# Performance work log

Hardware: AMD Instinct MI355X
Metric: run time of the kernel (lower is better)

The kernel has to match this reference:

```python
import jax, jax.numpy as jnp
import numpy as np

PATCH = 15  # patch_size (odd, per extract_patches arithmetic)


def _extract_patches(vol, centroids, P):
    """vol: (B,C,H,W,D) float; centroids: (B,N,3) int (x->H, y->W, z->D).
    Returns (B,N,C,P,P,P) with the valid region placed at the patch origin and
    zero padding at the high end of each axis (matches F.pad end-padding)."""
    B, C, H, Wd, D = vol.shape
    half = P // 2
    c = centroids.astype(jnp.int32)                      # (B,N,3)
    dims = jnp.array([H, Wd, D], dtype=jnp.int32)
    starts = jnp.maximum(c - half, 0)                    # (B,N,3)
    ends = jnp.minimum(c + half + 1, dims)               # (B,N,3)
    r = jnp.arange(P, dtype=jnp.int32)
    idx = starts[..., None] + r                          # (B,N,3,P)
    mask = idx < ends[..., None]                         # (B,N,3,P)
    idxc = jnp.minimum(idx, (dims - 1)[None, None, :, None])  # clamp for safe gather

    def one(vol_b, ix, iy, iz, m):
        # vol_b (C,H,W,D); ix/iy/iz (N,P); m (N,3,P)
        p = vol_b[:, ix[:, :, None, None], iy[:, None, :, None], iz[:, None, None, :]]
        p = jnp.transpose(p, (1, 0, 2, 3, 4))            # (N,C,P,P,P)
        m3 = (m[:, 0][:, :, None, None]
              & m[:, 1][:, None, :, None]
              & m[:, 2][:, None, None, :])               # (N,P,P,P)
        return jnp.where(m3[:, None], p, jnp.zeros((), vol_b.dtype))

    return jax.vmap(one)(vol, idxc[:, :, 0], idxc[:, :, 1], idxc[:, :, 2], mask)


def setup_inputs() -> dict:
    key = jax.random.key(0)
    k1, k2, k3 = jax.random.split(key, 3)
    B, C, H, W_, D = 2, 32, 96, 96, 96
    N, F = 64, 1024
    P = PATCH
    x = jax.random.normal(k1, (B, C, H, W_, D), dtype=jnp.float32)
    centroids = jax.random.randint(k2, (B, N, 3), 0, 96, dtype=jnp.int32)
    W = jax.random.normal(k3, (C * P ** 3, F), dtype=jnp.float32) * 0.01
    b = jnp.zeros((F,), dtype=jnp.float32)
    return {"x": x, "centroids": centroids, "W": W, "b": b}


def reference(x, centroids, W, b):
    P = PATCH
    patches = _extract_patches(x, centroids, P)          # (B,N,C,P,P,P)
    B, N = patches.shape[:2]
    flat = patches.reshape(B * N, -1)                    # (B*N, C*P^3)
    out = flat @ W + b                                   # feature_extraction_model
    return out.reshape(B, N, -1)
```

## Files before the change

### kernel.cpp

```cpp
#include <hip/hip_runtime.h>

typedef __attribute__((ext_vector_type(8))) __bf16 bf16x8;
typedef __attribute__((ext_vector_type(8))) unsigned short ushort8;
typedef __attribute__((ext_vector_type(4))) float f32x4;

constexpr int C_ = 32, NN = 64;
constexpr int PK = 3375;
constexpr int K_TOT = 108000;
constexpr int F_TOT = 1024;
constexpr int M_TOT = 128;
constexpr int KSTEPS = 3375;

constexpr int WPAIR  = 2064;
constexpr int WBUF   = 16 * WPAIR;
constexpr int ABUF   = 8192;
constexpr int RBUF   = WBUF + ABUF;

__device__ __forceinline__ unsigned short f2bf(float f) {
    unsigned int b = __builtin_bit_cast(unsigned int, f);
    b += 0x7FFFu + ((b >> 16) & 1u);
    return (unsigned short)(b >> 16);
}

__device__ __forceinline__ void async_copy16(void* lds, const void* g) {
    __builtin_amdgcn_global_load_lds(
        (const __attribute__((address_space(1))) unsigned int*)g,
        (__attribute__((address_space(3))) unsigned int*)lds, 16, 0, 0);
}

__global__ void extract_kernel(const float* __restrict__ x,
                               const int* __restrict__ cent,
                               unsigned short* __restrict__ Af) {
    int m = blockIdx.x;
    int c = blockIdx.y;
    int b = m >> 6, n = m & 63;
    int cx = cent[(b * NN + n) * 3 + 0];
    int cy = cent[(b * NN + n) * 3 + 1];
    int cz = cent[(b * NN + n) * 3 + 2];
    int sx = max(cx - 7, 0), ex = min(cx + 8, 96);
    int sy = max(cy - 7, 0), ey = min(cy + 8, 96);
    int sz = max(cz - 7, 0), ez = min(cz + 8, 96);
    const float* xb = x + (size_t)(b * C_ + c) * (96 * 96 * 96);
    unsigned short* Arow = Af + (size_t)m * K_TOT + (size_t)c * PK;
    for (int k = threadIdx.x; k < PK; k += blockDim.x) {
        int iz = k % 15;
        int t  = k / 15;
        int iy = t % 15;
        int ix = t / 15;
        int hx = sx + ix, wy = sy + iy, dz = sz + iz;
        float v = 0.0f;
        if (hx < ex && wy < ey && dz < ez)
            v = xb[(hx * 96 + wy) * 96 + dz];
        Arow[k] = f2bf(v);
    }
}

__global__ __launch_bounds__(256, 1) void gemm_kernel(const unsigned short* __restrict__ Af,
                                                      const float* __restrict__ W,
                                                      unsigned short* __restrict__ partial,
                                                      int CS) {
    __shared__ __align__(16) unsigned char smem[3 * RBUF];
    int s  = blockIdx.x;
    int fx = blockIdx.y;
    int st0 = s * CS;
    int st1 = min(st0 + CS, KSTEPS);
    int f0  = fx * 256;

    int tid  = (int)threadIdx.x;
    int wave = tid >> 6, lane = tid & 63;
    int fr = lane & 15, lgrp = lane >> 4;

    f32x4 acc[8][4];
#pragma unroll
    for (int i = 0; i < 8; ++i)
#pragma unroll
        for (int j = 0; j < 4; ++j) acc[i][j] = (f32x4)(0.0f);

    auto STAGE = [&](int buf, int st) {
        int k0 = st << 5;
        unsigned char* wb = smem + buf * RBUF;
        const float* wsrc = W + (size_t)k0 * F_TOT + f0 + (lane << 2);
#pragma unroll
        for (int r = 0; r < 8; ++r) {
            int row = r * 4 + wave;
            async_copy16(wb + (row >> 1) * WPAIR + (row & 1) * 1024,
                         wsrc + (size_t)row * F_TOT);
        }
        unsigned char* ab = wb + WBUF;
        const unsigned short* ag = Af + (size_t)fr * K_TOT + k0 + lgrp * 8;
#pragma unroll
        for (int i = 0; i < 2; ++i) {
            int mt = wave * 2 + i;
            async_copy16(ab + mt * 1024, ag + (size_t)(mt * 16) * K_TOT);
        }
    };

    auto COMPUTE = [&](int buf) {
        const unsigned char* wb = smem + buf * RBUF;
        const unsigned char* ab = wb + WBUF;
        bf16x8 afrag[8];
#pragma unroll
        for (int mt = 0; mt < 8; ++mt)
            afrag[mt] = *reinterpret_cast<const bf16x8*>(ab + mt * 1024 + lane * 16);
#pragma unroll
        for (int ft = 0; ft < 4; ++ft) {
            int fl4 = (wave * 64 + ft * 16 + fr) * 4;
            float wv[8];
#pragma unroll
            for (int j = 0; j < 8; ++j) {
                int row = lgrp * 8 + j;
                wv[j] = *reinterpret_cast<const float*>(
                            wb + (row >> 1) * WPAIR + (row & 1) * 1024 + fl4);
            }
            ushort8 bt;
#pragma unroll
            for (int j = 0; j < 8; ++j) bt[j] = f2bf(wv[j]);
            bf16x8 bfrag = __builtin_bit_cast(bf16x8, bt);
#pragma unroll
            for (int mt = 0; mt < 8; ++mt)
                acc[mt][ft] = __builtin_amdgcn_mfma_f32_16x16x32_bf16(afrag[mt], bfrag, acc[mt][ft], 0, 0, 0);
        }
    };

    int len = st1 - st0;
    STAGE(0, st0);
    if (len > 1) STAGE(1, st0 + 1);
    int t = st0, cb = 0;
    for (; t + 2 < st1; ++t) {
        int sb = cb + 2; if (sb >= 3) sb -= 3;
        STAGE(sb, t + 2);
        asm volatile("s_waitcnt vmcnt(20)" ::: "memory");
        __builtin_amdgcn_s_barrier();
        COMPUTE(cb);
        __builtin_amdgcn_s_barrier();
        if (++cb == 3) cb = 0;
    }
    if (t + 1 < st1) {
        asm volatile("s_waitcnt vmcnt(10)" ::: "memory");
        __builtin_amdgcn_s_barrier();
        COMPUTE(cb);
        __builtin_amdgcn_s_barrier();
        if (++cb == 3) cb = 0;
        ++t;
    }
    asm volatile("s_waitcnt vmcnt(0)" ::: "memory");
    __builtin_amdgcn_s_barrier();
    COMPUTE(cb);

    unsigned short* pout = partial + (size_t)s * (M_TOT * F_TOT);
#pragma unroll
    for (int mt = 0; mt < 8; ++mt) {
        int mbase = mt * 16 + lgrp * 4;
#pragma unroll
        for (int ft = 0; ft < 4; ++ft) {
            int f = f0 + wave * 64 + ft * 16 + fr;
#pragma unroll
            for (int r = 0; r < 4; ++r)
                pout[(size_t)(mbase + r) * F_TOT + f] = f2bf(acc[mt][ft][r]);
        }
    }
}

__global__ void reduce_kernel(const unsigned short* __restrict__ partial,
                              const float* __restrict__ bias,
                              float* __restrict__ out, int S) {
    int i8 = (blockIdx.x * blockDim.x + threadIdx.x) * 8;
    if (i8 >= M_TOT * F_TOT) return;
    float a[8];
#pragma unroll
    for (int j = 0; j < 8; ++j) a[j] = bias[(i8 & (F_TOT - 1)) + j];
    for (int s = 0; s < S; ++s) {
        ushort8 p = *reinterpret_cast<const ushort8*>(partial + (size_t)s * (M_TOT * F_TOT) + i8);
#pragma unroll
        for (int j = 0; j < 8; ++j)
            a[j] += __builtin_bit_cast(float, (unsigned int)p[j] << 16);
    }
#pragma unroll
    for (int j = 0; j < 8; ++j) out[i8 + j] = a[j];
}

extern "C" void kernel_launch(void* const* d_in, const int* in_sizes, int n_in,
                              void* d_out, int out_size, void* d_ws, size_t ws_size,
                              hipStream_t stream) {
    const float* x    = (const float*)d_in[0];
    const int*   cent = (const int*)d_in[1];
    const float* W    = (const float*)d_in[2];
    const float* bias = (const float*)d_in[3];
    float* out = (float*)d_out;

    unsigned short* Af = (unsigned short*)d_ws;
    size_t Af_bytes = (size_t)M_TOT * K_TOT * 2;
    unsigned short* partial = (unsigned short*)((char*)d_ws + Af_bytes);

    size_t avail = ws_size > Af_bytes ? ws_size - Af_bytes : 0;
    int S = (int)(avail / ((size_t)M_TOT * F_TOT * 2));
    if (S > 64) S = 64;
    if (S < 1)  S = 1;
    int CS = (KSTEPS + S - 1) / S;
    S = (KSTEPS + CS - 1) / CS;

    extract_kernel<<<dim3(M_TOT, C_), 256, 0, stream>>>(x, cent, Af);
    gemm_kernel<<<dim3(S, 4), 256, 0, stream>>>(Af, W, partial, CS);
    reduce_kernel<<<dim3((M_TOT * F_TOT) / (256 * 8)), 256, 0, stream>>>(partial, bias, out, S);
}
```

Measured before the change: 141.0 us.

## Store extracted patch matrix in K-blocked tiled layout for contiguous GEMM A loads

The extract kernel now writes the bf16 activation matrix in a K-octet-major layout (8 consecutive K values for all 128 rows stored contiguously), transposing through LDS. Each block handles 256 K columns across all 128 rows. The GEMM A staging then reads contiguous 16-byte chunks within a 1KB tile instead of rows strided by K_TOT. The aim is better coalescing of A loads in the GEMM, at the cost of a less coalesced gather in extract. The bias load in the reduce kernel is also vectorized.

```diff
diff --git a/kernel.cpp b/kernel.cpp
--- a/kernel.cpp
+++ b/kernel.cpp
@@ -28,11 +28,14 @@
         (__attribute__((address_space(3))) unsigned int*)lds, 16, 0, 0);
 }
 
-__global__ void extract_kernel(const float* __restrict__ x,
-                               const int* __restrict__ cent,
-                               unsigned short* __restrict__ Af) {
-    int m = blockIdx.x;
-    int c = blockIdx.y;
+__global__ __launch_bounds__(256) void extract_kernel(const float* __restrict__ x,
+                                                      const int* __restrict__ cent,
+                                                      unsigned short* __restrict__ A2) {
+    __shared__ unsigned short stage[256 * 128];
+    int K0   = blockIdx.x * 256;
+    int KLEN = min(256, K_TOT - K0);
+    int t = (int)threadIdx.x;
+    int m = t & 127, half = t >> 7;
     int b = m >> 6, n = m & 63;
     int cx = cent[(b * NN + n) * 3 + 0];
     int cy = cent[(b * NN + n) * 3 + 1];
@@ -40,22 +43,49 @@
     int sx = max(cx - 7, 0), ex = min(cx + 8, 96);
     int sy = max(cy - 7, 0), ey = min(cy + 8, 96);
     int sz = max(cz - 7, 0), ez = min(cz + 8, 96);
-    const float* xb = x + (size_t)(b * C_ + c) * (96 * 96 * 96);
-    unsigned short* Arow = Af + (size_t)m * K_TOT + (size_t)c * PK;
-    for (int k = threadIdx.x; k < PK; k += blockDim.x) {
-        int iz = k % 15;
-        int t  = k / 15;
-        int iy = t % 15;
-        int ix = t / 15;
-        int hx = sx + ix, wy = sy + iy, dz = sz + iz;
-        float v = 0.0f;
-        if (hx < ex && wy < ey && dz < ez)
-            v = xb[(hx * 96 + wy) * 96 + dz];
-        Arow[k] = f2bf(v);
-    }
-}
-
-__global__ __launch_bounds__(256, 1) void gemm_kernel(const unsigned short* __restrict__ Af,
+    int vx = ex - sx, vy = ey - sy, vz = ez - sz;
+    const float* xb = x + (size_t)(b * C_) * 884736 + ((sx * 96 + sy) * 96 + sz);
+
+    for (int i = 0; i < 16; ++i) {
+        float v[8];
+#pragma unroll
+        for (int j = 0; j < 8; ++j) {
+            int kk = half + 2 * (i * 8 + j);
+            v[j] = 0.0f;
+            if (kk < KLEN) {
+                int K  = K0 + kk;
+                int c  = K / 3375;
+                int kp = K - c * 3375;
+                int ix = kp / 225;
+                int r  = kp - ix * 225;
+                int iy = r / 15;
+                int iz = r - iy * 15;
+                if (ix < vx && iy < vy && iz < vz)
+                    v[j] = xb[(size_t)c * 884736 + ix * 9216 + iy * 96 + iz];
+            }
+        }
+#pragma unroll
+        for (int j = 0; j < 8; ++j) {
+            int kk = half + 2 * (i * 8 + j);
+            if (kk < KLEN) stage[kk * 128 + m] = f2bf(v[j]);
+        }
+    }
+    __syncthreads();
+
+    int span = (KLEN >> 3) * 1024;
+    unsigned short* outp = A2 + (size_t)(K0 >> 3) * 1024;
+    for (int idx = t * 8; idx < span; idx += 256 * 8) {
+        int o  = idx >> 10;
+        int mm = (idx >> 3) & 127;
+        ushort8 vv;
+#pragma unroll
+        for (int j = 0; j < 8; ++j)
+            vv[j] = stage[(o * 8 + j) * 128 + mm];
+        *reinterpret_cast<ushort8*>(outp + idx) = vv;
+    }
+}
+
+__global__ __launch_bounds__(256, 1) void gemm_kernel(const unsigned short* __restrict__ A2,
                                                       const float* __restrict__ W,
                                                       unsigned short* __restrict__ partial,
                                                       int CS) {
@@ -87,11 +117,11 @@
                          wsrc + (size_t)row * F_TOT);
         }
         unsigned char* ab = wb + WBUF;
-        const unsigned short* ag = Af + (size_t)fr * K_TOT + k0 + lgrp * 8;
+        const unsigned short* ag = A2 + ((size_t)(k0 >> 3) + lgrp) * 1024 + fr * 8;
 #pragma unroll
         for (int i = 0; i < 2; ++i) {
             int mt = wave * 2 + i;
-            async_copy16(ab + mt * 1024, ag + (size_t)(mt * 16) * K_TOT);
+            async_copy16(ab + mt * 1024, ag + mt * 128);
         }
     };
 
@@ -166,9 +196,9 @@
                               float* __restrict__ out, int S) {
     int i8 = (blockIdx.x * blockDim.x + threadIdx.x) * 8;
     if (i8 >= M_TOT * F_TOT) return;
-    float a[8];
-#pragma unroll
-    for (int j = 0; j < 8; ++j) a[j] = bias[(i8 & (F_TOT - 1)) + j];
+    f32x4 b0 = *reinterpret_cast<const f32x4*>(bias + (i8 & (F_TOT - 1)));
+    f32x4 b1 = *reinterpret_cast<const f32x4*>(bias + (i8 & (F_TOT - 1)) + 4);
+    float a[8] = {b0.x, b0.y, b0.z, b0.w, b1.x, b1.y, b1.z, b1.w};
     for (int s = 0; s < S; ++s) {
         ushort8 p = *reinterpret_cast<const ushort8*>(partial + (size_t)s * (M_TOT * F_TOT) + i8);
 #pragma unroll
@@ -188,18 +218,18 @@
     const float* bias = (const float*)d_in[3];
     float* out = (float*)d_out;
 
-    unsigned short* Af = (unsigned short*)d_ws;
-    size_t Af_bytes = (size_t)M_TOT * K_TOT * 2;
-    unsigned short* partial = (unsigned short*)((char*)d_ws + Af_bytes);
-
-    size_t avail = ws_size > Af_bytes ? ws_size - Af_bytes : 0;
+    unsigned short* A2 = (unsigned short*)d_ws;
+    size_t A2_bytes = (size_t)M_TOT * K_TOT * 2;
+    unsigned short* partial = (unsigned short*)((char*)d_ws + A2_bytes);
+
+    size_t avail = ws_size > A2_bytes ? ws_size - A2_bytes : 0;
     int S = (int)(avail / ((size_t)M_TOT * F_TOT * 2));
     if (S > 64) S = 64;
     if (S < 1)  S = 1;
     int CS = (KSTEPS + S - 1) / S;
     S = (KSTEPS + CS - 1) / CS;
 
-    extract_kernel<<<dim3(M_TOT, C_), 256, 0, stream>>>(x, cent, Af);
-    gemm_kernel<<<dim3(S, 4), 256, 0, stream>>>(Af, W, partial, CS);
+    extract_kernel<<<dim3((K_TOT + 255) / 256), 256, 0, stream>>>(x, cent, A2);
+    gemm_kernel<<<dim3(S, 4), 256, 0, stream>>>(A2, W, partial, CS);
     reduce_kernel<<<dim3((M_TOT * F_TOT) / (256 * 8)), 256, 0, stream>>>(partial, bias, out, S);
 }
```

After: 186.3 us. +32.1%, slower.

## Split GEMM block across 8 waves with M-halves and vectorize bias loads

Applied to the files above, without the earlier changes.

Raises the GEMM block from 4 to 8 waves. Each wave now owns half of the M tiles and one 64-column F slice, so per-wave accumulators drop from 32 to 16 MFMA tiles. Staging loads are redistributed across the 8 waves and the vmcnt thresholds are halved to match. This gives more waves per CU to hide LDS and global latency, but each wave must now convert the W fragments from fp32 to bf16 for only half as many MFMAs, so conversion work is duplicated. The reduce kernel also loads bias with vector loads.

```diff
diff --git a/kernel.cpp b/kernel.cpp
--- a/kernel.cpp
+++ b/kernel.cpp
@@ -55,7 +55,7 @@
     }
 }
 
-__global__ __launch_bounds__(256, 1) void gemm_kernel(const unsigned short* __restrict__ Af,
+__global__ __launch_bounds__(512, 1) void gemm_kernel(const unsigned short* __restrict__ Af,
                                                       const float* __restrict__ W,
                                                       unsigned short* __restrict__ partial,
                                                       int CS) {
@@ -69,10 +69,11 @@
     int tid  = (int)threadIdx.x;
     int wave = tid >> 6, lane = tid & 63;
     int fr = lane & 15, lgrp = lane >> 4;
-
-    f32x4 acc[8][4];
-#pragma unroll
-    for (int i = 0; i < 8; ++i)
+    int wh = wave >> 2, wf = wave & 3;
+
+    f32x4 acc[4][4];
+#pragma unroll
+    for (int i = 0; i < 4; ++i)
 #pragma unroll
         for (int j = 0; j < 4; ++j) acc[i][j] = (f32x4)(0.0f);
 
@@ -81,30 +82,26 @@
         unsigned char* wb = smem + buf * RBUF;
         const float* wsrc = W + (size_t)k0 * F_TOT + f0 + (lane << 2);
 #pragma unroll
-        for (int r = 0; r < 8; ++r) {
-            int row = r * 4 + wave;
+        for (int r = 0; r < 4; ++r) {
+            int row = r * 8 + wave;
             async_copy16(wb + (row >> 1) * WPAIR + (row & 1) * 1024,
                          wsrc + (size_t)row * F_TOT);
         }
         unsigned char* ab = wb + WBUF;
-        const unsigned short* ag = Af + (size_t)fr * K_TOT + k0 + lgrp * 8;
-#pragma unroll
-        for (int i = 0; i < 2; ++i) {
-            int mt = wave * 2 + i;
-            async_copy16(ab + mt * 1024, ag + (size_t)(mt * 16) * K_TOT);
-        }
+        const unsigned short* ag = Af + (size_t)(wave * 16 + fr) * K_TOT + k0 + lgrp * 8;
+        async_copy16(ab + wave * 1024, ag);
     };
 
     auto COMPUTE = [&](int buf) {
         const unsigned char* wb = smem + buf * RBUF;
         const unsigned char* ab = wb + WBUF;
-        bf16x8 afrag[8];
-#pragma unroll
-        for (int mt = 0; mt < 8; ++mt)
-            afrag[mt] = *reinterpret_cast<const bf16x8*>(ab + mt * 1024 + lane * 16);
+        bf16x8 afrag[4];
+#pragma unroll
+        for (int i = 0; i < 4; ++i)
+            afrag[i] = *reinterpret_cast<const bf16x8*>(ab + (wh * 4 + i) * 1024 + lane * 16);
 #pragma unroll
         for (int ft = 0; ft < 4; ++ft) {
-            int fl4 = (wave * 64 + ft * 16 + fr) * 4;
+            int fl4 = (wf * 64 + ft * 16 + fr) * 4;
             float wv[8];
 #pragma unroll
             for (int j = 0; j < 8; ++j) {
@@ -117,8 +114,8 @@
             for (int j = 0; j < 8; ++j) bt[j] = f2bf(wv[j]);
             bf16x8 bfrag = __builtin_bit_cast(bf16x8, bt);
 #pragma unroll
-            for (int mt = 0; mt < 8; ++mt)
-                acc[mt][ft] = __builtin_amdgcn_mfma_f32_16x16x32_bf16(afrag[mt], bfrag, acc[mt][ft], 0, 0, 0);
+            for (int i = 0; i < 4; ++i)
+                acc[i][ft] = __builtin_amdgcn_mfma_f32_16x16x32_bf16(afrag[i], bfrag, acc[i][ft], 0, 0, 0);
         }
     };
 
@@ -129,14 +126,14 @@
     for (; t + 2 < st1; ++t) {
         int sb = cb + 2; if (sb >= 3) sb -= 3;
         STAGE(sb, t + 2);
-        asm volatile("s_waitcnt vmcnt(20)" ::: "memory");
+        asm volatile("s_waitcnt vmcnt(10)" ::: "memory");
         __builtin_amdgcn_s_barrier();
         COMPUTE(cb);
         __builtin_amdgcn_s_barrier();
         if (++cb == 3) cb = 0;
     }
     if (t + 1 < st1) {
-        asm volatile("s_waitcnt vmcnt(10)" ::: "memory");
+        asm volatile("s_waitcnt vmcnt(5)" ::: "memory");
         __builtin_amdgcn_s_barrier();
         COMPUTE(cb);
         __builtin_amdgcn_s_barrier();
@@ -149,14 +146,14 @@
 
     unsigned short* pout = partial + (size_t)s * (M_TOT * F_TOT);
 #pragma unroll
-    for (int mt = 0; mt < 8; ++mt) {
-        int mbase = mt * 16 + lgrp * 4;
+    for (int i = 0; i < 4; ++i) {
+        int mbase = (wh * 4 + i) * 16 + lgrp * 4;
 #pragma unroll
         for (int ft = 0; ft < 4; ++ft) {
-            int f = f0 + wave * 64 + ft * 16 + fr;
+            int f = f0 + wf * 64 + ft * 16 + fr;
 #pragma unroll
             for (int r = 0; r < 4; ++r)
-                pout[(size_t)(mbase + r) * F_TOT + f] = f2bf(acc[mt][ft][r]);
+                pout[(size_t)(mbase + r) * F_TOT + f] = f2bf(acc[i][ft][r]);
         }
     }
 }
@@ -166,9 +163,9 @@
                               float* __restrict__ out, int S) {
     int i8 = (blockIdx.x * blockDim.x + threadIdx.x) * 8;
     if (i8 >= M_TOT * F_TOT) return;
-    float a[8];
-#pragma unroll
-    for (int j = 0; j < 8; ++j) a[j] = bias[(i8 & (F_TOT - 1)) + j];
+    f32x4 b0 = *reinterpret_cast<const f32x4*>(bias + (i8 & (F_TOT - 1)));
+    f32x4 b1 = *reinterpret_cast<const f32x4*>(bias + (i8 & (F_TOT - 1)) + 4);
+    float a[8] = {b0.x, b0.y, b0.z, b0.w, b1.x, b1.y, b1.z, b1.w};
     for (int s = 0; s < S; ++s) {
         ushort8 p = *reinterpret_cast<const ushort8*>(partial + (size_t)s * (M_TOT * F_TOT) + i8);
 #pragma unroll
@@ -200,6 +197,6 @@
     S = (KSTEPS + CS - 1) / CS;
 
     extract_kernel<<<dim3(M_TOT, C_), 256, 0, stream>>>(x, cent, Af);
-    gemm_kernel<<<dim3(S, 4), 256, 0, stream>>>(Af, W, partial, CS);
+    gemm_kernel<<<dim3(S, 4), 512, 0, stream>>>(Af, W, partial, CS);
     reduce_kernel<<<dim3((M_TOT * F_TOT) / (256 * 8)), 256, 0, stream>>>(partial, bias, out, S);
 }
```

Measured after the change: 139.4 us. No clear change (-1.2%).
